# Kernel optimization log

Hardware: AMD Instinct MI355X
Metric: run time of the kernel (lower is better)

Reference implementation:

```python
import jax, jax.numpy as jnp
import numpy as np

N_NODES = 50000
N_EDGES = 600000
D_IN = 128
DIMS = [128, 128, 128]
LEAKY_SLOPE = 0.01  # torch nn.LeakyReLU default


def setup_inputs() -> dict:
    key = jax.random.key(0)
    ks = jax.random.split(key, 10)
    feat = jax.random.uniform(ks[0], (N_NODES, D_IN), dtype=jnp.float32) + 1e-3
    edge_index = jax.random.randint(ks[1], (2, N_EDGES), 0, N_NODES, dtype=jnp.int64)
    edge_weight = jax.random.uniform(ks[2], (N_EDGES,), dtype=jnp.float32) + 1e-3
    # 3 GCNConv layers: x @ W ([c_in, c_out]) then scatter-aggregate, then + bias
    scale1 = 1.0 / np.sqrt(D_IN)
    W1 = jax.random.normal(ks[3], (D_IN, DIMS[0]), dtype=jnp.float32) * scale1
    b1 = jnp.zeros((DIMS[0],), dtype=jnp.float32)
    W2 = jax.random.normal(ks[4], (DIMS[0], DIMS[1]), dtype=jnp.float32) * (1.0 / np.sqrt(DIMS[0]))
    b2 = jnp.zeros((DIMS[1],), dtype=jnp.float32)
    W3 = jax.random.normal(ks[5], (DIMS[1], DIMS[2]), dtype=jnp.float32) * (1.0 / np.sqrt(DIMS[1]))
    b3 = jnp.zeros((DIMS[2],), dtype=jnp.float32)
    return {"feat": feat, "edge_index": edge_index, "edge_weight": edge_weight,
            "W1": W1, "b1": b1, "W2": W2, "b2": b2, "W3": W3, "b3": b3}


def reference(feat, edge_index, edge_weight, W1, b1, W2, b2, W3, b3):
    N = feat.shape[0]
    src = edge_index[0]  # edge (i, j): A[i, j]; messages flow src -> dst
    dst = edge_index[1]
    # A_hat = D^{-1} A D^{-1}, D = diag(row sums of A)
    rowsum = jax.ops.segment_sum(edge_weight, src, num_segments=N)
    rinv = jnp.where(rowsum > 0, 1.0 / rowsum, 0.0)
    w_hat = edge_weight * rinv[src] * rinv[dst]
    # PyG gcn_norm (add_self_loops=False): deg over target, symmetric D^{-1/2} scaling
    deg = jax.ops.segment_sum(w_hat, dst, num_segments=N)
    dinv = jnp.where(deg > 0, jax.lax.rsqrt(deg), 0.0)
    norm = dinv[src] * w_hat * dinv[dst]  # cached, shared by all layers

    def gcn_conv(x, W, b):
        x = x @ W                              # [N, c_out]
        msg = norm[:, None] * x[src]           # gather + scale: [E, c_out]
        agg = jax.ops.segment_sum(msg, dst, num_segments=N)  # scatter-add
        return agg + b

    x = feat / jnp.sum(feat, axis=1, keepdims=True)  # row-normalize
    x = jax.nn.leaky_relu(gcn_conv(x, W1, b1), LEAKY_SLOPE)
    x = jax.nn.leaky_relu(gcn_conv(x, W2, b2), LEAKY_SLOPE)
    x = gcn_conv(x, W3, b3)  # final layer: no activation
    return x
```

## Files before the change

### kernel.cpp

```cpp
#include <hip/hip_runtime.h>

#define D 128
#define LEAKY 0.01f
#define SCAN_CHUNK 2048

typedef __attribute__((ext_vector_type(8))) short short8;
typedef __attribute__((ext_vector_type(4))) float f32x4;

__device__ __forceinline__ unsigned short f2bf(float f) {
    unsigned u = __float_as_uint(f);
    u += 0x7fffu + ((u >> 16) & 1u);
    return (unsigned short)(u >> 16);
}


__global__ void k_pass1(const int* __restrict__ src, const int* __restrict__ dst,
                        const float* __restrict__ w, float* __restrict__ rowsum,
                        int* __restrict__ cnt, int* __restrict__ rank, int E) {
    int e = blockIdx.x * 256 + threadIdx.x;
    if (e >= E) return;
    atomicAdd(&rowsum[src[e]], w[e]);
    rank[e] = atomicAdd(&cnt[dst[e]], 1);
}


__global__ void k_chunk_sum(const int* __restrict__ cnt, int* __restrict__ partial, int n) {
    __shared__ int sdata[256];
    int b = blockIdx.x;
    int base = b * SCAN_CHUNK;
    int s = 0;
    for (int i = threadIdx.x; i < SCAN_CHUNK; i += 256) {
        int idx = base + i;
        s += (idx < n) ? cnt[idx] : 0;
    }
    sdata[threadIdx.x] = s;
    __syncthreads();
    for (int off = 128; off > 0; off >>= 1) {
        if (threadIdx.x < off) sdata[threadIdx.x] += sdata[threadIdx.x + off];
        __syncthreads();
    }
    if (threadIdx.x == 0) partial[b] = sdata[0];
}

__global__ void k_scan_partial(int* __restrict__ partial, int nchunks) {
    if (blockIdx.x == 0 && threadIdx.x == 0) {
        int run = 0;
        for (int i = 0; i < nchunks; i++) { int v = partial[i]; partial[i] = run; run += v; }
    }
}

__global__ void k_chunk_scan(const int* __restrict__ cnt, const int* __restrict__ partial,
                             int* __restrict__ start, int n, int total) {
    __shared__ int sdata[256];
    int b = blockIdx.x;
    int base = b * SCAN_CHUNK;
    int t = threadIdx.x;
    int loc[8];
    int s = 0;
    int tb = base + t * 8;
    #pragma unroll
    for (int j = 0; j < 8; j++) {
        int idx = tb + j;
        int v = (idx < n) ? cnt[idx] : 0;
        loc[j] = s;
        s += v;
    }
    sdata[t] = s;
    __syncthreads();
    for (int off = 1; off < 256; off <<= 1) {
        int v = (t >= off) ? sdata[t - off] : 0;
        __syncthreads();
        sdata[t] += v;
        __syncthreads();
    }
    int texcl = (t == 0) ? 0 : sdata[t - 1];
    int offb = partial[b];
    #pragma unroll
    for (int j = 0; j < 8; j++) {
        int idx = tb + j;
        if (idx < n) start[idx] = offb + texcl + loc[j];
    }
    if (b == gridDim.x - 1 && t == 255) start[n] = total;
}


__global__ void k_scatter2(const int* __restrict__ src, const int* __restrict__ dst,
                           const float* __restrict__ w, const float* __restrict__ rowsum,
                           const int* __restrict__ start, const int* __restrict__ rank,
                           int2* __restrict__ csr, int E) {
    int e = blockIdx.x * 256 + threadIdx.x;
    if (e >= E) return;
    int s = src[e], d = dst[e];
    float rs = rowsum[s], rd = rowsum[d];
    float wh = w[e] * (rs > 0.f ? 1.f / rs : 0.f) * (rd > 0.f ? 1.f / rd : 0.f);
    int idx = start[d] + rank[e];
    csr[idx] = make_int2(s, __float_as_int(wh));
}


__global__ void k_deg_dinv(const int2* __restrict__ csr, const int* __restrict__ start,
                           float* __restrict__ dinv, int N) {
    int n = blockIdx.x * 256 + threadIdx.x;
    if (n >= N) return;
    int s0 = start[n], s1 = start[n + 1];
    float s = 0.f;
    for (int i = s0; i < s1; i++) s += __int_as_float(csr[i].y);
    dinv[n] = s > 0.f ? rsqrtf(s) : 0.f;
}


__global__ void k_csr_norm(int2* __restrict__ csr, const int* __restrict__ start,
                           const float* __restrict__ dinv, int N) {
    int g = (blockIdx.x * blockDim.x + threadIdx.x) >> 4;
    int l = threadIdx.x & 15;
    if (g >= N) return;
    int s0 = start[g], s1 = start[g + 1];
    float dd = dinv[g];
    for (int i = s0 + l; i < s1; i += 16) {
        int2 p = csr[i];
        float nm = __int_as_float(p.y) * dinv[p.x] * dd;
        csr[i] = make_int2(p.x, __float_as_int(nm));
    }
}


__global__ void k_norm_feat(const float* __restrict__ feat, unsigned short* __restrict__ xb,
                            int N) {
    int node = (blockIdx.x * blockDim.x + threadIdx.x) >> 6;
    int lane = threadIdx.x & 63;
    if (node >= N) return;
    const float* f = feat + (size_t)node * D;
    float a = f[lane], b = f[lane + 64];
    float s = a + b;
    #pragma unroll
    for (int off = 32; off > 0; off >>= 1) s += __shfl_down(s, off);
    s = __shfl(s, 0);
    float inv = 1.0f / s;
    xb[(size_t)node * D + lane] = f2bf(a * inv);
    xb[(size_t)node * D + 64 + lane] = f2bf(b * inv);
}


#define GR 64

__global__ __launch_bounds__(256) void k_gemm_mfma(const unsigned short* __restrict__ Xb,
                                                   const float* __restrict__ W,
                                                   unsigned short* __restrict__ Yb, int nrows) {
    __shared__ unsigned short Wt[128 * 128];
    __shared__ unsigned short Xs[GR * 128];
    int t = threadIdx.x;

    for (int i = t; i < 128 * 128; i += 256) {
        int k = i >> 7, col = i & 127;
        unsigned short h = f2bf(W[i]);
        int byte = col * 256 + ((k * 2) ^ ((col & 7) << 4));
        *(unsigned short*)((char*)Wt + byte) = h;
    }
    int rowbase = blockIdx.x * GR;
    for (int i = t; i < GR * 16; i += 256) {
        int r = i >> 4, c = i & 15;
        uint4 v = {0u, 0u, 0u, 0u};
        int row = rowbase + r;
        if (row < nrows) v = *(const uint4*)(Xb + (size_t)row * 128 + c * 8);
        int byte = r * 256 + ((c * 16) ^ ((r & 7) << 4));
        *(uint4*)((char*)Xs + byte) = v;
    }
    __syncthreads();

    int w = t >> 6, l = t & 63;
    int r0 = w * 16;
    int lr = l & 15, lg = l >> 4;

    short8 a[4];
    {
        int row = r0 + lr;
        const char* rp = (const char*)Xs + row * 256;
        int sw = (row & 7) << 4;
        #pragma unroll
        for (int s = 0; s < 4; s++)
            a[s] = *(const short8*)(rp + ((s * 64 + lg * 16) ^ sw));
    }

    f32x4 acc[8];
    #pragma unroll
    for (int ct = 0; ct < 8; ct++) {
        f32x4 c = {0.f, 0.f, 0.f, 0.f};
        int col = ct * 16 + lr;
        const char* cp = (const char*)Wt + col * 256;
        int sw = (col & 7) << 4;
        #pragma unroll
        for (int s = 0; s < 4; s++) {
            short8 b = *(const short8*)(cp + ((s * 64 + lg * 16) ^ sw));
            c = __builtin_amdgcn_mfma_f32_16x16x32_bf16(a[s], b, c, 0, 0, 0);
        }
        acc[ct] = c;
    }

    #pragma unroll
    for (int j = 0; j < 4; j++) {
        int row = rowbase + r0 + lg * 4 + j;
        if (row < nrows) {
            #pragma unroll
            for (int ct = 0; ct < 8; ct++)
                Yb[(size_t)row * 128 + ct * 16 + lr] = f2bf(acc[ct][j]);
        }
    }
}


__device__ __forceinline__ void fma_row(float4& acc, float n, uint2 v) {
    acc.x += n * __uint_as_float(v.x << 16);
    acc.y += n * __uint_as_float(v.x & 0xffff0000u);
    acc.z += n * __uint_as_float(v.y << 16);
    acc.w += n * __uint_as_float(v.y & 0xffff0000u);
}

__global__ void k_agg(const unsigned short* __restrict__ Yb, const int2* __restrict__ csr,
                      const int* __restrict__ start, const float* __restrict__ bias,
                      unsigned short* __restrict__ OutB, float* __restrict__ OutF,
                      int final_, int N) {
    int wid = (blockIdx.x * blockDim.x + threadIdx.x) >> 6;
    int lane = threadIdx.x & 63;
    int half = lane >> 5;
    int l = lane & 31;
    int node = wid * 2 + half;
    bool valid = node < N;
    int s0 = valid ? start[node] : 0;
    int s1 = valid ? start[node + 1] : 0;
    int cnt = s1 - s0;

    float4 acc = {0.f, 0.f, 0.f, 0.f};
    const uint2* Y2 = (const uint2*)Yb;

    for (int base = 0; base < cnt; base += 32) {
        int rem = cnt - base; if (rem > 32) rem = 32;
        int2 pr = (l < rem) ? csr[s0 + base + l] : make_int2(0, 0);
        int  sj = pr.x;
        float nj = __int_as_float(pr.y);
        int j = 0;
        for (; j + 8 <= rem; j += 8) {
            int   i0 = __shfl(sj, j + 0, 32), i1 = __shfl(sj, j + 1, 32);
            int   i2 = __shfl(sj, j + 2, 32), i3 = __shfl(sj, j + 3, 32);
            int   i4 = __shfl(sj, j + 4, 32), i5 = __shfl(sj, j + 5, 32);
            int   i6 = __shfl(sj, j + 6, 32), i7 = __shfl(sj, j + 7, 32);
            float n0 = __shfl(nj, j + 0, 32), n1 = __shfl(nj, j + 1, 32);
            float n2 = __shfl(nj, j + 2, 32), n3 = __shfl(nj, j + 3, 32);
            float n4 = __shfl(nj, j + 4, 32), n5 = __shfl(nj, j + 5, 32);
            float n6 = __shfl(nj, j + 6, 32), n7 = __shfl(nj, j + 7, 32);
            uint2 v0 = Y2[(size_t)i0 * 32 + l];
            uint2 v1 = Y2[(size_t)i1 * 32 + l];
            uint2 v2 = Y2[(size_t)i2 * 32 + l];
            uint2 v3 = Y2[(size_t)i3 * 32 + l];
            uint2 v4 = Y2[(size_t)i4 * 32 + l];
            uint2 v5 = Y2[(size_t)i5 * 32 + l];
            uint2 v6 = Y2[(size_t)i6 * 32 + l];
            uint2 v7 = Y2[(size_t)i7 * 32 + l];
            fma_row(acc, n0, v0); fma_row(acc, n1, v1);
            fma_row(acc, n2, v2); fma_row(acc, n3, v3);
            fma_row(acc, n4, v4); fma_row(acc, n5, v5);
            fma_row(acc, n6, v6); fma_row(acc, n7, v7);
        }
        for (; j + 4 <= rem; j += 4) {
            int   i0 = __shfl(sj, j + 0, 32), i1 = __shfl(sj, j + 1, 32);
            int   i2 = __shfl(sj, j + 2, 32), i3 = __shfl(sj, j + 3, 32);
            float n0 = __shfl(nj, j + 0, 32), n1 = __shfl(nj, j + 1, 32);
            float n2 = __shfl(nj, j + 2, 32), n3 = __shfl(nj, j + 3, 32);
            uint2 v0 = Y2[(size_t)i0 * 32 + l];
            uint2 v1 = Y2[(size_t)i1 * 32 + l];
            uint2 v2 = Y2[(size_t)i2 * 32 + l];
            uint2 v3 = Y2[(size_t)i3 * 32 + l];
            fma_row(acc, n0, v0); fma_row(acc, n1, v1);
            fma_row(acc, n2, v2); fma_row(acc, n3, v3);
        }
        for (; j < rem; j++) {
            int   i0 = __shfl(sj, j, 32);
            float n0 = __shfl(nj, j, 32);
            uint2 v0 = Y2[(size_t)i0 * 32 + l];
            fma_row(acc, n0, v0);
        }
    }

    if (!valid) return;
    float4 b4 = ((const float4*)bias)[l];
    float4 v;
    v.x = acc.x + b4.x; v.y = acc.y + b4.y; v.z = acc.z + b4.z; v.w = acc.w + b4.w;
    if (final_) {
        ((float4*)OutF)[(size_t)node * 32 + l] = v;
    } else {
        v.x = v.x > 0.f ? v.x : LEAKY * v.x;
        v.y = v.y > 0.f ? v.y : LEAKY * v.y;
        v.z = v.z > 0.f ? v.z : LEAKY * v.z;
        v.w = v.w > 0.f ? v.w : LEAKY * v.w;
        uint2 o;
        o.x = (unsigned)f2bf(v.x) | ((unsigned)f2bf(v.y) << 16);
        o.y = (unsigned)f2bf(v.z) | ((unsigned)f2bf(v.w) << 16);
        ((uint2*)OutB)[(size_t)node * 32 + l] = o;
    }
}


extern "C" void kernel_launch(void* const* d_in, const int* in_sizes, int n_in,
                              void* d_out, int out_size, void* d_ws, size_t ws_size,
                              hipStream_t stream) {
    const float* feat = (const float*)d_in[0];
    const int*   eidx = (const int*)d_in[1];
    const float* ew   = (const float*)d_in[2];
    const float* W1   = (const float*)d_in[3];
    const float* b1   = (const float*)d_in[4];
    const float* W2   = (const float*)d_in[5];
    const float* b2   = (const float*)d_in[6];
    const float* W3   = (const float*)d_in[7];
    const float* b3   = (const float*)d_in[8];

    const int N = in_sizes[0] / D;
    const int E = in_sizes[2];
    const int* src = eidx;
    const int* dst = eidx + E;

    size_t off = 0;
    char* base = (char*)d_ws;
    auto alloc4 = [&](size_t elems) -> void* {
        void* p = base + off * 4;
        off += (elems + 3) & ~(size_t)3;
        return p;
    };
    float* rowsum = (float*)alloc4(N);
    int*   cnt    = (int*)  alloc4(N);
    char*  zero_end = base + off * 4;
    int*   start  = (int*)  alloc4(N + 1);
    float* dinv   = (float*)alloc4(N);
    int*   partial= (int*)  alloc4(64);
    int*   rank   = (int*)  alloc4(E);
    int2*  csr    = (int2*) alloc4((size_t)E * 2);
    unsigned short* xb = (unsigned short*)alloc4((size_t)N * 64);
    unsigned short* yb = (unsigned short*)alloc4((size_t)N * 64);
    float* outp = (float*)d_out;

    hipMemsetAsync(rowsum, 0, (size_t)(zero_end - (char*)rowsum), stream);

    int eblocks = (E + 255) / 256;
    int nchunks = (N + SCAN_CHUNK - 1) / SCAN_CHUNK;
    int nblocks = (N + 255) / 256;
    int cblocks = ((size_t)N * 16 + 255) / 256;
    int ablocks = ((N + 1) / 2 * 64 + 255) / 256;
    int wblocks = (N + 3) / 4;
    int gblocks = (N + GR - 1) / GR;

    k_pass1<<<eblocks, 256, 0, stream>>>(src, dst, ew, rowsum, cnt, rank, E);

    k_chunk_sum<<<nchunks, 256, 0, stream>>>(cnt, partial, N);
    k_scan_partial<<<1, 64, 0, stream>>>(partial, nchunks);
    k_chunk_scan<<<nchunks, 256, 0, stream>>>(cnt, partial, start, N, E);

    k_scatter2<<<eblocks, 256, 0, stream>>>(src, dst, ew, rowsum, start, rank, csr, E);
    k_deg_dinv<<<nblocks, 256, 0, stream>>>(csr, start, dinv, N);
    k_csr_norm<<<cblocks, 256, 0, stream>>>(csr, start, dinv, N);

    k_norm_feat<<<wblocks, 256, 0, stream>>>(feat, xb, N);

    k_gemm_mfma<<<gblocks, 256, 0, stream>>>(xb, W1, xb, N);
    k_agg<<<ablocks, 256, 0, stream>>>(xb, csr, start, b1, yb, nullptr, 0, N);
    k_gemm_mfma<<<gblocks, 256, 0, stream>>>(yb, W2, yb, N);
    k_agg<<<ablocks, 256, 0, stream>>>(yb, csr, start, b2, xb, nullptr, 0, N);
    k_gemm_mfma<<<gblocks, 256, 0, stream>>>(xb, W3, xb, N);
    k_agg<<<ablocks, 256, 0, stream>>>(xb, csr, start, b3, nullptr, outp, 1, N);
}
```

Baseline: 335.7 us.

## Fuse feature row-normalization into first GEMM and widen aggregation loads

Removes the separate row-normalization kernel by having the first MFMA GEMM load fp32 features, compute each row sum with a 4-lane shuffle reduction, and write normalized bf16 into shared memory. This drops one launch and one bf16 write/read of the node features. The aggregation kernel now handles four nodes per wavefront with 16 lanes each loading 16 bytes per neighbor row, instead of two nodes with 32 lanes loading 8 bytes. That widens gather transactions and adds per-wave parallelism at the cost of more accumulator registers. A zero row sum now yields zero rather than inf.

New measurement: 333.8 us. About the same (-0.6%).

```diff
diff --git a/kernel.cpp b/kernel.cpp
--- a/kernel.cpp
+++ b/kernel.cpp
@@ -124,31 +124,17 @@
 }
 
 
-__global__ void k_norm_feat(const float* __restrict__ feat, unsigned short* __restrict__ xb,
-                            int N) {
-    int node = (blockIdx.x * blockDim.x + threadIdx.x) >> 6;
-    int lane = threadIdx.x & 63;
-    if (node >= N) return;
-    const float* f = feat + (size_t)node * D;
-    float a = f[lane], b = f[lane + 64];
-    float s = a + b;
-    #pragma unroll
-    for (int off = 32; off > 0; off >>= 1) s += __shfl_down(s, off);
-    s = __shfl(s, 0);
-    float inv = 1.0f / s;
-    xb[(size_t)node * D + lane] = f2bf(a * inv);
-    xb[(size_t)node * D + 64 + lane] = f2bf(b * inv);
-}
-
-
 #define GR 64
 
-__global__ __launch_bounds__(256) void k_gemm_mfma(const unsigned short* __restrict__ Xb,
+template<int DO_NORM>
+__global__ __launch_bounds__(256) void k_gemm_mfma(const float* __restrict__ Xf32,
+                                                   const unsigned short* __restrict__ Xb,
                                                    const float* __restrict__ W,
                                                    unsigned short* __restrict__ Yb, int nrows) {
     __shared__ unsigned short Wt[128 * 128];
     __shared__ unsigned short Xs[GR * 128];
     int t = threadIdx.x;
+    int rowbase = blockIdx.x * GR;
 
     for (int i = t; i < 128 * 128; i += 256) {
         int k = i >> 7, col = i & 127;
@@ -156,14 +142,42 @@
         int byte = col * 256 + ((k * 2) ^ ((col & 7) << 4));
         *(unsigned short*)((char*)Wt + byte) = h;
     }
-    int rowbase = blockIdx.x * GR;
-    for (int i = t; i < GR * 16; i += 256) {
-        int r = i >> 4, c = i & 15;
-        uint4 v = {0u, 0u, 0u, 0u};
+
+    if (DO_NORM) {
+        int r = t >> 2, q = t & 3;
         int row = rowbase + r;
-        if (row < nrows) v = *(const uint4*)(Xb + (size_t)row * 128 + c * 8);
-        int byte = r * 256 + ((c * 16) ^ ((r & 7) << 4));
-        *(uint4*)((char*)Xs + byte) = v;
+        const float4* Xr = (const float4*)(Xf32 + (size_t)row * 128);
+        float4 v[8];
+        float s = 0.f;
+        #pragma unroll
+        for (int k = 0; k < 8; k++) {
+            float4 x = make_float4(0.f, 0.f, 0.f, 0.f);
+            if (row < nrows) x = Xr[q + k * 4];
+            v[k] = x;
+            s += x.x + x.y + x.z + x.w;
+        }
+        s += __shfl_down(s, 2, 4);
+        s += __shfl_down(s, 1, 4);
+        float tot = __shfl(s, 0, 4);
+        float inv = tot > 0.f ? 1.f / tot : 0.f;
+        int sw = (r & 7) << 4;
+        #pragma unroll
+        for (int k = 0; k < 8; k++) {
+            int gidx = q + k * 4;
+            ushort4 h;
+            h.x = f2bf(v[k].x * inv); h.y = f2bf(v[k].y * inv);
+            h.z = f2bf(v[k].z * inv); h.w = f2bf(v[k].w * inv);
+            *(ushort4*)((char*)Xs + r * 256 + ((gidx * 8) ^ sw)) = h;
+        }
+    } else {
+        for (int i = t; i < GR * 16; i += 256) {
+            int r = i >> 4, c = i & 15;
+            uint4 vv = {0u, 0u, 0u, 0u};
+            int row = rowbase + r;
+            if (row < nrows) vv = *(const uint4*)(Xb + (size_t)row * 128 + c * 8);
+            int byte = r * 256 + ((c * 16) ^ ((r & 7) << 4));
+            *(uint4*)((char*)Xs + byte) = vv;
+        }
     }
     __syncthreads();
 
@@ -208,11 +222,15 @@
 }
 
 
-__device__ __forceinline__ void fma_row(float4& acc, float n, uint2 v) {
-    acc.x += n * __uint_as_float(v.x << 16);
-    acc.y += n * __uint_as_float(v.x & 0xffff0000u);
-    acc.z += n * __uint_as_float(v.y << 16);
-    acc.w += n * __uint_as_float(v.y & 0xffff0000u);
+__device__ __forceinline__ void fma8(float* acc, float n, uint4 v) {
+    acc[0] += n * __uint_as_float(v.x << 16);
+    acc[1] += n * __uint_as_float(v.x & 0xffff0000u);
+    acc[2] += n * __uint_as_float(v.y << 16);
+    acc[3] += n * __uint_as_float(v.y & 0xffff0000u);
+    acc[4] += n * __uint_as_float(v.z << 16);
+    acc[5] += n * __uint_as_float(v.z & 0xffff0000u);
+    acc[6] += n * __uint_as_float(v.w << 16);
+    acc[7] += n * __uint_as_float(v.w & 0xffff0000u);
 }
 
 __global__ void k_agg(const unsigned short* __restrict__ Yb, const int2* __restrict__ csr,
@@ -221,80 +239,85 @@
                       int final_, int N) {
     int wid = (blockIdx.x * blockDim.x + threadIdx.x) >> 6;
     int lane = threadIdx.x & 63;
-    int half = lane >> 5;
-    int l = lane & 31;
-    int node = wid * 2 + half;
+    int g = lane >> 4;
+    int l = lane & 15;
+    int node = wid * 4 + g;
     bool valid = node < N;
     int s0 = valid ? start[node] : 0;
     int s1 = valid ? start[node + 1] : 0;
     int cnt = s1 - s0;
 
-    float4 acc = {0.f, 0.f, 0.f, 0.f};
-    const uint2* Y2 = (const uint2*)Yb;
-
-    for (int base = 0; base < cnt; base += 32) {
-        int rem = cnt - base; if (rem > 32) rem = 32;
+    float acc[8] = {};
+    const uint4* Y4 = (const uint4*)Yb;
+
+    for (int base = 0; base < cnt; base += 16) {
+        int rem = cnt - base; if (rem > 16) rem = 16;
         int2 pr = (l < rem) ? csr[s0 + base + l] : make_int2(0, 0);
         int  sj = pr.x;
         float nj = __int_as_float(pr.y);
         int j = 0;
         for (; j + 8 <= rem; j += 8) {
-            int   i0 = __shfl(sj, j + 0, 32), i1 = __shfl(sj, j + 1, 32);
-            int   i2 = __shfl(sj, j + 2, 32), i3 = __shfl(sj, j + 3, 32);
-            int   i4 = __shfl(sj, j + 4, 32), i5 = __shfl(sj, j + 5, 32);
-            int   i6 = __shfl(sj, j + 6, 32), i7 = __shfl(sj, j + 7, 32);
-            float n0 = __shfl(nj, j + 0, 32), n1 = __shfl(nj, j + 1, 32);
-            float n2 = __shfl(nj, j + 2, 32), n3 = __shfl(nj, j + 3, 32);
-            float n4 = __shfl(nj, j + 4, 32), n5 = __shfl(nj, j + 5, 32);
-            float n6 = __shfl(nj, j + 6, 32), n7 = __shfl(nj, j + 7, 32);
-            uint2 v0 = Y2[(size_t)i0 * 32 + l];
-            uint2 v1 = Y2[(size_t)i1 * 32 + l];
-            uint2 v2 = Y2[(size_t)i2 * 32 + l];
-            uint2 v3 = Y2[(size_t)i3 * 32 + l];
-            uint2 v4 = Y2[(size_t)i4 * 32 + l];
-            uint2 v5 = Y2[(size_t)i5 * 32 + l];
-            uint2 v6 = Y2[(size_t)i6 * 32 + l];
-            uint2 v7 = Y2[(size_t)i7 * 32 + l];
-            fma_row(acc, n0, v0); fma_row(acc, n1, v1);
-            fma_row(acc, n2, v2); fma_row(acc, n3, v3);
-            fma_row(acc, n4, v4); fma_row(acc, n5, v5);
-            fma_row(acc, n6, v6); fma_row(acc, n7, v7);
+            int   i0 = __shfl(sj, j + 0, 16), i1 = __shfl(sj, j + 1, 16);
+            int   i2 = __shfl(sj, j + 2, 16), i3 = __shfl(sj, j + 3, 16);
+            int   i4 = __shfl(sj, j + 4, 16), i5 = __shfl(sj, j + 5, 16);
+            int   i6 = __shfl(sj, j + 6, 16), i7 = __shfl(sj, j + 7, 16);
+            float n0 = __shfl(nj, j + 0, 16), n1 = __shfl(nj, j + 1, 16);
+            float n2 = __shfl(nj, j + 2, 16), n3 = __shfl(nj, j + 3, 16);
+            float n4 = __shfl(nj, j + 4, 16), n5 = __shfl(nj, j + 5, 16);
+            float n6 = __shfl(nj, j + 6, 16), n7 = __shfl(nj, j + 7, 16);
+            uint4 v0 = Y4[(size_t)i0 * 16 + l];
+            uint4 v1 = Y4[(size_t)i1 * 16 + l];
+            uint4 v2 = Y4[(size_t)i2 * 16 + l];
+            uint4 v3 = Y4[(size_t)i3 * 16 + l];
+            uint4 v4 = Y4[(size_t)i4 * 16 + l];
+            uint4 v5 = Y4[(size_t)i5 * 16 + l];
+            uint4 v6 = Y4[(size_t)i6 * 16 + l];
+            uint4 v7 = Y4[(size_t)i7 * 16 + l];
+            fma8(acc, n0, v0); fma8(acc, n1, v1);
+            fma8(acc, n2, v2); fma8(acc, n3, v3);
+            fma8(acc, n4, v4); fma8(acc, n5, v5);
+            fma8(acc, n6, v6); fma8(acc, n7, v7);
         }
         for (; j + 4 <= rem; j += 4) {
-            int   i0 = __shfl(sj, j + 0, 32), i1 = __shfl(sj, j + 1, 32);
-            int   i2 = __shfl(sj, j + 2, 32), i3 = __shfl(sj, j + 3, 32);
-            float n0 = __shfl(nj, j + 0, 32), n1 = __shfl(nj, j + 1, 32);
-            float n2 = __shfl(nj, j + 2, 32), n3 = __shfl(nj, j + 3, 32);
-            uint2 v0 = Y2[(size_t)i0 * 32 + l];
-            uint2 v1 = Y2[(size_t)i1 * 32 + l];
-            uint2 v2 = Y2[(size_t)i2 * 32 + l];
-            uint2 v3 = Y2[(size_t)i3 * 32 + l];
-            fma_row(acc, n0, v0); fma_row(acc, n1, v1);
-            fma_row(acc, n2, v2); fma_row(acc, n3, v3);
+            int   i0 = __shfl(sj, j + 0, 16), i1 = __shfl(sj, j + 1, 16);
+            int   i2 = __shfl(sj, j + 2, 16), i3 = __shfl(sj, j + 3, 16);
+            float n0 = __shfl(nj, j + 0, 16), n1 = __shfl(nj, j + 1, 16);
+            float n2 = __shfl(nj, j + 2, 16), n3 = __shfl(nj, j + 3, 16);
+            uint4 v0 = Y4[(size_t)i0 * 16 + l];
+            uint4 v1 = Y4[(size_t)i1 * 16 + l];
+            uint4 v2 = Y4[(size_t)i2 * 16 + l];
+            uint4 v3 = Y4[(size_t)i3 * 16 + l];
+            fma8(acc, n0, v0); fma8(acc, n1, v1);
+            fma8(acc, n2, v2); fma8(acc, n3, v3);
         }
         for (; j < rem; j++) {
-            int   i0 = __shfl(sj, j, 32);
-            float n0 = __shfl(nj, j, 32);
-            uint2 v0 = Y2[(size_t)i0 * 32 + l];
-            fma_row(acc, n0, v0);
+            int   i0 = __shfl(sj, j, 16);
+            float n0 = __shfl(nj, j, 16);
+            uint4 v0 = Y4[(size_t)i0 * 16 + l];
+            fma8(acc, n0, v0);
         }
     }
 
     if (!valid) return;
-    float4 b4 = ((const float4*)bias)[l];
-    float4 v;
-    v.x = acc.x + b4.x; v.y = acc.y + b4.y; v.z = acc.z + b4.z; v.w = acc.w + b4.w;
+    float4 ba = ((const float4*)bias)[l * 2];
+    float4 bb = ((const float4*)bias)[l * 2 + 1];
+    float o[8];
+    o[0] = acc[0] + ba.x; o[1] = acc[1] + ba.y; o[2] = acc[2] + ba.z; o[3] = acc[3] + ba.w;
+    o[4] = acc[4] + bb.x; o[5] = acc[5] + bb.y; o[6] = acc[6] + bb.z; o[7] = acc[7] + bb.w;
     if (final_) {
-        ((float4*)OutF)[(size_t)node * 32 + l] = v;
+        float4 w0 = {o[0], o[1], o[2], o[3]};
+        float4 w1 = {o[4], o[5], o[6], o[7]};
+        ((float4*)OutF)[(size_t)node * 32 + l * 2] = w0;
+        ((float4*)OutF)[(size_t)node * 32 + l * 2 + 1] = w1;
     } else {
-        v.x = v.x > 0.f ? v.x : LEAKY * v.x;
-        v.y = v.y > 0.f ? v.y : LEAKY * v.y;
-        v.z = v.z > 0.f ? v.z : LEAKY * v.z;
-        v.w = v.w > 0.f ? v.w : LEAKY * v.w;
-        uint2 o;
-        o.x = (unsigned)f2bf(v.x) | ((unsigned)f2bf(v.y) << 16);
-        o.y = (unsigned)f2bf(v.z) | ((unsigned)f2bf(v.w) << 16);
-        ((uint2*)OutB)[(size_t)node * 32 + l] = o;
+        #pragma unroll
+        for (int k = 0; k < 8; k++) o[k] = o[k] > 0.f ? o[k] : LEAKY * o[k];
+        uint4 ov;
+        ov.x = (unsigned)f2bf(o[0]) | ((unsigned)f2bf(o[1]) << 16);
+        ov.y = (unsigned)f2bf(o[2]) | ((unsigned)f2bf(o[3]) << 16);
+        ov.z = (unsigned)f2bf(o[4]) | ((unsigned)f2bf(o[5]) << 16);
+        ov.w = (unsigned)f2bf(o[6]) | ((unsigned)f2bf(o[7]) << 16);
+        ((uint4*)OutB)[(size_t)node * 16 + l] = ov;
     }
 }
 
@@ -342,8 +365,7 @@
     int nchunks = (N + SCAN_CHUNK - 1) / SCAN_CHUNK;
     int nblocks = (N + 255) / 256;
     int cblocks = ((size_t)N * 16 + 255) / 256;
-    int ablocks = ((N + 1) / 2 * 64 + 255) / 256;
-    int wblocks = (N + 3) / 4;
+    int ablocks = (((N + 3) / 4) * 64 + 255) / 256;
     int gblocks = (N + GR - 1) / GR;
 
     k_pass1<<<eblocks, 256, 0, stream>>>(src, dst, ew, rowsum, cnt, rank, E);
@@ -356,12 +378,10 @@
     k_deg_dinv<<<nblocks, 256, 0, stream>>>(csr, start, dinv, N);
     k_csr_norm<<<cblocks, 256, 0, stream>>>(csr, start, dinv, N);
 
-    k_norm_feat<<<wblocks, 256, 0, stream>>>(feat, xb, N);
-
-    k_gemm_mfma<<<gblocks, 256, 0, stream>>>(xb, W1, xb, N);
+    k_gemm_mfma<1><<<gblocks, 256, 0, stream>>>(feat, nullptr, W1, xb, N);
     k_agg<<<ablocks, 256, 0, stream>>>(xb, csr, start, b1, yb, nullptr, 0, N);
-    k_gemm_mfma<<<gblocks, 256, 0, stream>>>(yb, W2, yb, N);
+    k_gemm_mfma<0><<<gblocks, 256, 0, stream>>>(nullptr, yb, W2, yb, N);
     k_agg<<<ablocks, 256, 0, stream>>>(yb, csr, start, b2, xb, nullptr, 0, N);
-    k_gemm_mfma<<<gblocks, 256, 0, stream>>>(xb, W3, xb, N);
+    k_gemm_mfma<0><<<gblocks, 256, 0, stream>>>(nullptr, xb, W3, xb, N);
     k_agg<<<ablocks, 256, 0, stream>>>(xb, csr, start, b3, nullptr, outp, 1, N);
 }
```
